# Kernel tuning notes

Hardware: AMD Instinct MI355X
Metric: run time of the kernel (lower is better)

Reference implementation:

```python
import jax, jax.numpy as jnp
import numpy as np

N_NODES = 10000
N_EDGES = 640000
D_FEAT = 128


def setup_inputs() -> dict:
    key = jax.random.key(0)
    k1, k2, k3, k4 = jax.random.split(key, 4)
    feat = jax.random.normal(k1, (N_NODES, D_FEAT), dtype=jnp.float32)
    src = jax.random.randint(k2, (N_EDGES,), 0, N_NODES, dtype=jnp.int32)
    dst = jax.random.randint(k3, (N_EDGES,), 0, N_NODES, dtype=jnp.int32)
    W = jax.random.normal(k4, (D_FEAT, D_FEAT), dtype=jnp.float32) / np.sqrt(D_FEAT).astype(np.float32)
    b = jnp.zeros((D_FEAT,), dtype=jnp.float32)
    return {"feat": feat, "W": W, "b": b, "src": src, "dst": dst}


def reference(feat, W, b, src, dst):
    eps = jnp.float32(0.0)  # init_eps=0, learn_eps=False (buffer)
    n = feat.shape[0]
    # message passing: copy_u('h','m') + sum reducer -> neigh[i] = sum_{j->i} h_j
    h_src = feat[src]                                   # [E, D] gather
    neigh = jax.ops.segment_sum(h_src, dst, num_segments=n)  # [N, D] scatter-add
    rst = (1.0 + eps) * feat + neigh
    # apply_func: Linear(D, D)
    rst = rst @ W + b
    # per-edge score: e = sum(h_src * tanh(h_dst), axis=1)
    e = jnp.sum(h_src * jnp.tanh(feat[dst]), axis=1)    # [E]
    # edge_softmax: softmax over edges grouped by destination node
    m = jax.ops.segment_max(e, dst, num_segments=n)     # [N]
    e_exp = jnp.exp(e - m[dst])
    denom = jax.ops.segment_sum(e_exp, dst, num_segments=n)  # [N]
    e_soft = e_exp / denom[dst]
    return rst, e_soft
```

## Files before the change

### kernel.cpp

```cpp
#include <hip/hip_runtime.h>
#include <hip/hip_bf16.h>
#include <math.h>

#define N_NODES 10000
#define N_EDGES 640000
#define D_FEAT  128
#define SLOT    128


__global__ void scatter_build(const int* __restrict__ src,
                              const int* __restrict__ dst,
                              int* __restrict__ cnt,
                              unsigned short* __restrict__ slot_us,
                              int* __restrict__ pos_by_edge) {
    int i = blockIdx.x * 256 + threadIdx.x;
    int d = dst[i];
    int pos = atomicAdd(&cnt[d], 1);
    int idx = d * SLOT + pos;
    slot_us[idx] = (unsigned short)src[i];
    pos_by_edge[i] = idx;
}

__global__ void fused_node(const float* __restrict__ feat,
                           const int* __restrict__ cnt,
                           const unsigned short* __restrict__ slot_us,
                           float* __restrict__ e_slot,
                           float* __restrict__ x_out) {
    __shared__ float t_sh[4][D_FEAT];
    __shared__ float e_sh[4][SLOT];
    int wv = threadIdx.x >> 6;
    int lane = threadIdx.x & 63;
    int node = blockIdx.x * 4 + wv;
    if (node >= N_NODES) return;

    int g = lane >> 4;
    int l = lane & 15;

    int deg = cnt[node];
    unsigned base = (unsigned)node * SLOT;

    float2 fd2 = ((const float2*)(feat + (size_t)node * D_FEAT))[lane];
    ((float2*)&t_sh[wv][0])[lane] = make_float2(tanhf(fd2.x), tanhf(fd2.y));
    float4 t0 = ((const float4*)&t_sh[wv][0])[l * 2];
    float4 t1 = ((const float4*)&t_sh[wv][0])[l * 2 + 1];

    float4 acc0 = make_float4(0.f, 0.f, 0.f, 0.f);
    float4 acc1 = make_float4(0.f, 0.f, 0.f, 0.f);

    for (int cbase = 0; cbase < deg; cbase += 64) {
        int n = min(64, deg - cbase);
        int my_src = (int)slot_us[base + min(cbase + lane, deg - 1)];
        int j = 0;
        for (; j + 8 <= n; j += 8) {
            int s0 = __shfl(my_src, j + g, 64);
            int s1 = __shfl(my_src, j + 4 + g, 64);
            const float4* r0 = (const float4*)(feat + (size_t)s0 * D_FEAT) + l * 2;
            const float4* r1 = (const float4*)(feat + (size_t)s1 * D_FEAT) + l * 2;
            float4 v00 = r0[0], v01 = r0[1];
            float4 v10 = r1[0], v11 = r1[1];
            acc0.x += v00.x + v10.x; acc0.y += v00.y + v10.y;
            acc0.z += v00.z + v10.z; acc0.w += v00.w + v10.w;
            acc1.x += v01.x + v11.x; acc1.y += v01.y + v11.y;
            acc1.z += v01.z + v11.z; acc1.w += v01.w + v11.w;
            float d0 = v00.x * t0.x + v00.y * t0.y + v00.z * t0.z + v00.w * t0.w
                     + v01.x * t1.x + v01.y * t1.y + v01.z * t1.z + v01.w * t1.w;
            float d1 = v10.x * t0.x + v10.y * t0.y + v10.z * t0.z + v10.w * t0.w
                     + v11.x * t1.x + v11.y * t1.y + v11.z * t1.z + v11.w * t1.w;
            #pragma unroll
            for (int off = 1; off <= 8; off <<= 1) {
                d0 += __shfl_xor(d0, off, 64);
                d1 += __shfl_xor(d1, off, 64);
            }
            if (l == 0) {
                e_sh[wv][cbase + j + g] = d0;
                e_sh[wv][cbase + j + 4 + g] = d1;
            }
        }
        for (; j < n; j += 4) {
            int idx = j + g;
            bool act = idx < n;
            int s = __shfl(my_src, min(idx, n - 1), 64);
            const float4* r0 = (const float4*)(feat + (size_t)s * D_FEAT) + l * 2;
            float4 v0 = r0[0], v1 = r0[1];
            if (!act) {
                v0 = make_float4(0.f, 0.f, 0.f, 0.f);
                v1 = make_float4(0.f, 0.f, 0.f, 0.f);
            }
            acc0.x += v0.x; acc0.y += v0.y; acc0.z += v0.z; acc0.w += v0.w;
            acc1.x += v1.x; acc1.y += v1.y; acc1.z += v1.z; acc1.w += v1.w;
            float d = v0.x * t0.x + v0.y * t0.y + v0.z * t0.z + v0.w * t0.w
                    + v1.x * t1.x + v1.y * t1.y + v1.z * t1.z + v1.w * t1.w;
            #pragma unroll
            for (int off = 1; off <= 8; off <<= 1)
                d += __shfl_xor(d, off, 64);
            if (act && l == 0) e_sh[wv][cbase + idx] = d;
        }
    }

    #pragma unroll
    for (int off = 16; off <= 32; off <<= 1) {
        acc0.x += __shfl_xor(acc0.x, off, 64);
        acc0.y += __shfl_xor(acc0.y, off, 64);
        acc0.z += __shfl_xor(acc0.z, off, 64);
        acc0.w += __shfl_xor(acc0.w, off, 64);
        acc1.x += __shfl_xor(acc1.x, off, 64);
        acc1.y += __shfl_xor(acc1.y, off, 64);
        acc1.z += __shfl_xor(acc1.z, off, 64);
        acc1.w += __shfl_xor(acc1.w, off, 64);
    }

    float2 mp = (g == 0) ? make_float2(acc0.x, acc0.y)
              : (g == 1) ? make_float2(acc0.z, acc0.w)
              : (g == 2) ? make_float2(acc1.x, acc1.y)
              :            make_float2(acc1.z, acc1.w);
    int p2 = l * 4 + g;
    float2 fn = ((const float2*)(feat + (size_t)node * D_FEAT))[p2];
    ((float2*)(x_out + (size_t)node * D_FEAT))[p2] =
        make_float2(mp.x + fn.x, mp.y + fn.y);

    float mx = -INFINITY;
    for (int i = lane; i < deg; i += 64) mx = fmaxf(mx, e_sh[wv][i]);
    #pragma unroll
    for (int off = 32; off; off >>= 1)
        mx = fmaxf(mx, __shfl_xor(mx, off, 64));

    float sum = 0.f;
    for (int i = lane; i < deg; i += 64) {
        float ex = expf(e_sh[wv][i] - mx);
        e_sh[wv][i] = ex;
        sum += ex;
    }
    #pragma unroll
    for (int off = 32; off; off >>= 1)
        sum += __shfl_xor(sum, off, 64);

    float inv = 1.0f / sum;
    for (int i = lane; i < deg; i += 64)
        e_slot[base + i] = e_sh[wv][i] * inv;
}

__global__ void gemm_and_edge(float* __restrict__ io,
                              const float* __restrict__ W,
                              const float* __restrict__ b,
                              const int* __restrict__ pos_by_edge,
                              const float* __restrict__ e_slot,
                              float* __restrict__ out_e) {
    if (blockIdx.x >= 625) {
        int i4 = ((blockIdx.x - 625) * 256 + threadIdx.x) * 4;
        int4 p = *(const int4*)&pos_by_edge[i4];
        float4 r;
        r.x = e_slot[p.x];
        r.y = e_slot[p.y];
        r.z = e_slot[p.z];
        r.w = e_slot[p.w];
        *(float4*)&out_e[i4] = r;
        return;
    }

    __shared__ float xst[D_FEAT][20];
    int rbase = blockIdx.x * 16;

    for (int i = threadIdx.x; i < 16 * D_FEAT; i += 256) {
        int r = i >> 7, c = i & 127;
        xst[c][r] = io[(size_t)(rbase + r) * D_FEAT + c];
    }
    __syncthreads();

    int col = threadIdx.x & 127;
    int rh  = threadIdx.x >> 7;
    float acc[8] = {0.f, 0.f, 0.f, 0.f, 0.f, 0.f, 0.f, 0.f};

    for (int k = 0; k < D_FEAT; ++k) {
        float4 xa = *(const float4*)&xst[k][rh * 8];
        float4 xb = *(const float4*)&xst[k][rh * 8 + 4];
        float wk = W[(size_t)k * D_FEAT + col];
        acc[0] += xa.x * wk; acc[1] += xa.y * wk;
        acc[2] += xa.z * wk; acc[3] += xa.w * wk;
        acc[4] += xb.x * wk; acc[5] += xb.y * wk;
        acc[6] += xb.z * wk; acc[7] += xb.w * wk;
    }
    __syncthreads();

    float bias = b[col];
    #pragma unroll
    for (int r = 0; r < 8; ++r)
        io[(size_t)(rbase + rh * 8 + r) * D_FEAT + col] = acc[r] + bias;
}

extern "C" void kernel_launch(void* const* d_in, const int* in_sizes, int n_in,
                              void* d_out, int out_size, void* d_ws, size_t ws_size,
                              hipStream_t stream) {
    const float* feat = (const float*)d_in[0];
    const float* W    = (const float*)d_in[1];
    const float* b    = (const float*)d_in[2];
    const int*   src  = (const int*)d_in[3];
    const int*   dst  = (const int*)d_in[4];

    float* out_rst = (float*)d_out;
    float* out_e   = (float*)d_out + (size_t)N_NODES * D_FEAT;

    char* ws = (char*)d_ws;
    int*            cnt         = (int*)(ws + 0);
    unsigned short* slot_us     = (unsigned short*)(ws + 65536);
    float*          e_slot      = (float*)(ws + 2686976);
    int*            pos_by_edge = (int*)(ws + 7806976);

    hipMemsetAsync(cnt, 0, N_NODES * sizeof(int), stream);

    scatter_build<<<N_EDGES / 256, 256, 0, stream>>>(src, dst, cnt, slot_us, pos_by_edge);

    fused_node<<<(N_NODES + 3) / 4, 256, 0, stream>>>(feat, cnt, slot_us, e_slot, out_rst);

    gemm_and_edge<<<1250, 256, 0, stream>>>(out_rst, W, b, pos_by_edge, e_slot, out_e);
}
```

Baseline: 148.2 us.

## Pad atomic counters, vectorize scatter build, prefetch gathers, retile GEMM

Counters are padded to one per 64 bytes so atomics on different nodes stop sharing cache lines, and the scatter build now handles four edges per thread with vectorized loads. The node kernel loads up to 128 source indices up front and software-pipelines the feature-row gathers, issuing the next step's loads before processing the current one. The GEMM is retiled to a 4x2 register block per thread with float2 loads of W and float2 stores. These changes add register pressure and a larger memset, and the node kernel now assumes degree is at most 128.

```diff
diff --git a/kernel.cpp b/kernel.cpp
--- a/kernel.cpp
+++ b/kernel.cpp
@@ -6,6 +6,7 @@
 #define N_EDGES 640000
 #define D_FEAT  128
 #define SLOT    128
+#define MAXDEG  128
 
 
 __global__ void scatter_build(const int* __restrict__ src,
@@ -13,12 +14,23 @@
                               int* __restrict__ cnt,
                               unsigned short* __restrict__ slot_us,
                               int* __restrict__ pos_by_edge) {
-    int i = blockIdx.x * 256 + threadIdx.x;
-    int d = dst[i];
-    int pos = atomicAdd(&cnt[d], 1);
-    int idx = d * SLOT + pos;
-    slot_us[idx] = (unsigned short)src[i];
-    pos_by_edge[i] = idx;
+    int i0 = (blockIdx.x * 256 + threadIdx.x) * 4;
+    int4 s4 = *(const int4*)&src[i0];
+    int4 d4 = *(const int4*)&dst[i0];
+    int p0 = atomicAdd(&cnt[d4.x << 4], 1);
+    int p1 = atomicAdd(&cnt[d4.y << 4], 1);
+    int p2 = atomicAdd(&cnt[d4.z << 4], 1);
+    int p3 = atomicAdd(&cnt[d4.w << 4], 1);
+    int4 q;
+    q.x = d4.x * SLOT + p0;
+    q.y = d4.y * SLOT + p1;
+    q.z = d4.z * SLOT + p2;
+    q.w = d4.w * SLOT + p3;
+    slot_us[q.x] = (unsigned short)s4.x;
+    slot_us[q.y] = (unsigned short)s4.y;
+    slot_us[q.z] = (unsigned short)s4.z;
+    slot_us[q.w] = (unsigned short)s4.w;
+    *(int4*)&pos_by_edge[i0] = q;
 }
 
 __global__ void fused_node(const float* __restrict__ feat,
@@ -27,7 +39,7 @@
                            float* __restrict__ e_slot,
                            float* __restrict__ x_out) {
     __shared__ float t_sh[4][D_FEAT];
-    __shared__ float e_sh[4][SLOT];
+    __shared__ float e_sh[4][MAXDEG];
     int wv = threadIdx.x >> 6;
     int lane = threadIdx.x & 63;
     int node = blockIdx.x * 4 + wv;
@@ -36,7 +48,8 @@
     int g = lane >> 4;
     int l = lane & 15;
 
-    int deg = cnt[node];
+    int deg = cnt[node << 4];
+    int dm = (deg > 0) ? deg - 1 : 0;
     unsigned base = (unsigned)node * SLOT;
 
     float2 fd2 = ((const float2*)(feat + (size_t)node * D_FEAT))[lane];
@@ -44,58 +57,80 @@
     float4 t0 = ((const float4*)&t_sh[wv][0])[l * 2];
     float4 t1 = ((const float4*)&t_sh[wv][0])[l * 2 + 1];
 
+    int m0 = (int)slot_us[base + min(lane, dm)];
+    int m1 = (int)slot_us[base + min(64 + lane, dm)];
+
     float4 acc0 = make_float4(0.f, 0.f, 0.f, 0.f);
     float4 acc1 = make_float4(0.f, 0.f, 0.f, 0.f);
 
-    for (int cbase = 0; cbase < deg; cbase += 64) {
-        int n = min(64, deg - cbase);
-        int my_src = (int)slot_us[base + min(cbase + lane, deg - 1)];
-        int j = 0;
-        for (; j + 8 <= n; j += 8) {
-            int s0 = __shfl(my_src, j + g, 64);
-            int s1 = __shfl(my_src, j + 4 + g, 64);
-            const float4* r0 = (const float4*)(feat + (size_t)s0 * D_FEAT) + l * 2;
-            const float4* r1 = (const float4*)(feat + (size_t)s1 * D_FEAT) + l * 2;
-            float4 v00 = r0[0], v01 = r0[1];
-            float4 v10 = r1[0], v11 = r1[1];
-            acc0.x += v00.x + v10.x; acc0.y += v00.y + v10.y;
-            acc0.z += v00.z + v10.z; acc0.w += v00.w + v10.w;
-            acc1.x += v01.x + v11.x; acc1.y += v01.y + v11.y;
-            acc1.z += v01.z + v11.z; acc1.w += v01.w + v11.w;
-            float d0 = v00.x * t0.x + v00.y * t0.y + v00.z * t0.z + v00.w * t0.w
-                     + v01.x * t1.x + v01.y * t1.y + v01.z * t1.z + v01.w * t1.w;
-            float d1 = v10.x * t0.x + v10.y * t0.y + v10.z * t0.z + v10.w * t0.w
-                     + v11.x * t1.x + v11.y * t1.y + v11.z * t1.z + v11.w * t1.w;
+    int nsteps = (deg + 7) >> 3;
+
+    float4 Va0, Va1, Va2, Va3;
+    #define LOAD_STEP(T, V0, V1, V2, V3)                                      \
+        {                                                                     \
+            int m_ = ((T) < 8) ? m0 : m1;                                     \
+            int s0_ = __shfl(m_, ((T) * 8 + g) & 63, 64);                     \
+            int s1_ = __shfl(m_, ((T) * 8 + 4 + g) & 63, 64);                 \
+            const float4* r0_ = (const float4*)(feat + (size_t)s0_ * D_FEAT) + l * 2; \
+            const float4* r1_ = (const float4*)(feat + (size_t)s1_ * D_FEAT) + l * 2; \
+            V0 = r0_[0]; V1 = r0_[1]; V2 = r1_[0]; V3 = r1_[1];               \
+        }
+
+    if (nsteps > 0) LOAD_STEP(0, Va0, Va1, Va2, Va3);
+
+    for (int t = 0; t < nsteps; ++t) {
+        float4 Vb0 = Va0, Vb1 = Va1, Vb2 = Va2, Vb3 = Va3;
+        if (t + 1 < nsteps) LOAD_STEP(t + 1, Vb0, Vb1, Vb2, Vb3);
+
+        int i0 = t * 8 + g;
+        int i1 = i0 + 4;
+        if (((t + 1) << 3) <= deg) {
+            acc0.x += Va0.x + Va2.x; acc0.y += Va0.y + Va2.y;
+            acc0.z += Va0.z + Va2.z; acc0.w += Va0.w + Va2.w;
+            acc1.x += Va1.x + Va3.x; acc1.y += Va1.y + Va3.y;
+            acc1.z += Va1.z + Va3.z; acc1.w += Va1.w + Va3.w;
+            float d0 = Va0.x * t0.x + Va0.y * t0.y + Va0.z * t0.z + Va0.w * t0.w
+                     + Va1.x * t1.x + Va1.y * t1.y + Va1.z * t1.z + Va1.w * t1.w;
+            float d1 = Va2.x * t0.x + Va2.y * t0.y + Va2.z * t0.z + Va2.w * t0.w
+                     + Va3.x * t1.x + Va3.y * t1.y + Va3.z * t1.z + Va3.w * t1.w;
             #pragma unroll
             for (int off = 1; off <= 8; off <<= 1) {
                 d0 += __shfl_xor(d0, off, 64);
                 d1 += __shfl_xor(d1, off, 64);
             }
             if (l == 0) {
-                e_sh[wv][cbase + j + g] = d0;
-                e_sh[wv][cbase + j + 4 + g] = d1;
-            }
+                e_sh[wv][i0] = d0;
+                e_sh[wv][i1] = d1;
+            }
+        } else {
+            bool a0 = i0 < deg, a1 = i1 < deg;
+            if (!a0) {
+                Va0 = make_float4(0.f, 0.f, 0.f, 0.f);
+                Va1 = make_float4(0.f, 0.f, 0.f, 0.f);
+            }
+            if (!a1) {
+                Va2 = make_float4(0.f, 0.f, 0.f, 0.f);
+                Va3 = make_float4(0.f, 0.f, 0.f, 0.f);
+            }
+            acc0.x += Va0.x + Va2.x; acc0.y += Va0.y + Va2.y;
+            acc0.z += Va0.z + Va2.z; acc0.w += Va0.w + Va2.w;
+            acc1.x += Va1.x + Va3.x; acc1.y += Va1.y + Va3.y;
+            acc1.z += Va1.z + Va3.z; acc1.w += Va1.w + Va3.w;
+            float d0 = Va0.x * t0.x + Va0.y * t0.y + Va0.z * t0.z + Va0.w * t0.w
+                     + Va1.x * t1.x + Va1.y * t1.y + Va1.z * t1.z + Va1.w * t1.w;
+            float d1 = Va2.x * t0.x + Va2.y * t0.y + Va2.z * t0.z + Va2.w * t0.w
+                     + Va3.x * t1.x + Va3.y * t1.y + Va3.z * t1.z + Va3.w * t1.w;
+            #pragma unroll
+            for (int off = 1; off <= 8; off <<= 1) {
+                d0 += __shfl_xor(d0, off, 64);
+                d1 += __shfl_xor(d1, off, 64);
+            }
+            if (a0 && l == 0) e_sh[wv][i0] = d0;
+            if (a1 && l == 0) e_sh[wv][i1] = d1;
         }
-        for (; j < n; j += 4) {
-            int idx = j + g;
-            bool act = idx < n;
-            int s = __shfl(my_src, min(idx, n - 1), 64);
-            const float4* r0 = (const float4*)(feat + (size_t)s * D_FEAT) + l * 2;
-            float4 v0 = r0[0], v1 = r0[1];
-            if (!act) {
-                v0 = make_float4(0.f, 0.f, 0.f, 0.f);
-                v1 = make_float4(0.f, 0.f, 0.f, 0.f);
-            }
-            acc0.x += v0.x; acc0.y += v0.y; acc0.z += v0.z; acc0.w += v0.w;
-            acc1.x += v1.x; acc1.y += v1.y; acc1.z += v1.z; acc1.w += v1.w;
-            float d = v0.x * t0.x + v0.y * t0.y + v0.z * t0.z + v0.w * t0.w
-                    + v1.x * t1.x + v1.y * t1.y + v1.z * t1.z + v1.w * t1.w;
-            #pragma unroll
-            for (int off = 1; off <= 8; off <<= 1)
-                d += __shfl_xor(d, off, 64);
-            if (act && l == 0) e_sh[wv][cbase + idx] = d;
-        }
-    }
+        Va0 = Vb0; Va1 = Vb1; Va2 = Vb2; Va3 = Vb3;
+    }
+    #undef LOAD_STEP
 
     #pragma unroll
     for (int off = 16; off <= 32; off <<= 1) {
@@ -166,25 +201,28 @@
     }
     __syncthreads();
 
-    int col = threadIdx.x & 127;
-    int rh  = threadIdx.x >> 7;
-    float acc[8] = {0.f, 0.f, 0.f, 0.f, 0.f, 0.f, 0.f, 0.f};
+    int tc = threadIdx.x & 63;
+    int rh = threadIdx.x >> 6;
+    float a00 = 0.f, a01 = 0.f, a10 = 0.f, a11 = 0.f;
+    float a20 = 0.f, a21 = 0.f, a30 = 0.f, a31 = 0.f;
 
     for (int k = 0; k < D_FEAT; ++k) {
-        float4 xa = *(const float4*)&xst[k][rh * 8];
-        float4 xb = *(const float4*)&xst[k][rh * 8 + 4];
-        float wk = W[(size_t)k * D_FEAT + col];
-        acc[0] += xa.x * wk; acc[1] += xa.y * wk;
-        acc[2] += xa.z * wk; acc[3] += xa.w * wk;
-        acc[4] += xb.x * wk; acc[5] += xb.y * wk;
-        acc[6] += xb.z * wk; acc[7] += xb.w * wk;
+        float2 xa = *(const float2*)&xst[k][rh * 4];
+        float2 xb = *(const float2*)&xst[k][rh * 4 + 2];
+        float2 w  = *(const float2*)&W[(size_t)k * D_FEAT + tc * 2];
+        a00 += xa.x * w.x; a01 += xa.x * w.y;
+        a10 += xa.y * w.x; a11 += xa.y * w.y;
+        a20 += xb.x * w.x; a21 += xb.x * w.y;
+        a30 += xb.y * w.x; a31 += xb.y * w.y;
     }
     __syncthreads();
 
-    float bias = b[col];
-    #pragma unroll
-    for (int r = 0; r < 8; ++r)
-        io[(size_t)(rbase + rh * 8 + r) * D_FEAT + col] = acc[r] + bias;
+    float2 bias = *(const float2*)&b[tc * 2];
+    int rw = rbase + rh * 4;
+    ((float2*)&io[(size_t)(rw + 0) * D_FEAT])[tc] = make_float2(a00 + bias.x, a01 + bias.y);
+    ((float2*)&io[(size_t)(rw + 1) * D_FEAT])[tc] = make_float2(a10 + bias.x, a11 + bias.y);
+    ((float2*)&io[(size_t)(rw + 2) * D_FEAT])[tc] = make_float2(a20 + bias.x, a21 + bias.y);
+    ((float2*)&io[(size_t)(rw + 3) * D_FEAT])[tc] = make_float2(a30 + bias.x, a31 + bias.y);
 }
 
 extern "C" void kernel_launch(void* const* d_in, const int* in_sizes, int n_in,
@@ -201,13 +239,13 @@
 
     char* ws = (char*)d_ws;
     int*            cnt         = (int*)(ws + 0);
-    unsigned short* slot_us     = (unsigned short*)(ws + 65536);
-    float*          e_slot      = (float*)(ws + 2686976);
-    int*            pos_by_edge = (int*)(ws + 7806976);
-
-    hipMemsetAsync(cnt, 0, N_NODES * sizeof(int), stream);
-
-    scatter_build<<<N_EDGES / 256, 256, 0, stream>>>(src, dst, cnt, slot_us, pos_by_edge);
+    unsigned short* slot_us     = (unsigned short*)(ws + 640000);
+    float*          e_slot      = (float*)(ws + 3200000);
+    int*            pos_by_edge = (int*)(ws + 8320000);
+
+    hipMemsetAsync(cnt, 0, 640000, stream);
+
+    scatter_build<<<N_EDGES / 4 / 256, 256, 0, stream>>>(src, dst, cnt, slot_us, pos_by_edge);
 
     fused_node<<<(N_NODES + 3) / 4, 256, 0, stream>>>(feat, cnt, slot_us, e_slot, out_rst);
 
```

New measurement: 141.0 us. 1.05x faster.
